# Kernel optimization log

Measured on AMD Instinct MI355X. Metric: run time of the kernel, lower is better.

Reference implementation:

```python
import jax, jax.numpy as jnp
import numpy as np

B, N, DIM, DD = 8, 4096, 512, 512
SCALE = DD ** -0.5


def setup_inputs() -> dict:
    key = jax.random.key(0)
    ks = jax.random.split(key, 8)
    x = jax.random.normal(ks[0], (B, N, DIM), dtype=jnp.float32)
    mask = jnp.ones((B, N), dtype=bool)
    # torch nn.Linear(dim, decode_dim, bias=False): weight [DD, DIM], y = x @ W.T
    Wq = jax.random.normal(ks[1], (DD, DIM), dtype=jnp.float32) * (DIM ** -0.5)
    Wk = jax.random.normal(ks[2], (DD, DIM), dtype=jnp.float32) * (DIM ** -0.5)
    Wv = jax.random.normal(ks[3], (DD, DIM), dtype=jnp.float32) * (DIM ** -0.5)
    Wr = jax.random.normal(ks[4], (DD, DD), dtype=jnp.float32) * (DD ** -0.5)
    w_alpha = jax.random.normal(ks[5], (DD,), dtype=jnp.float32)
    w_beta = jax.random.normal(ks[6], (DD,), dtype=jnp.float32)
    return {"x": x, "Wq": Wq, "Wk": Wk, "Wv": Wv, "Wr": Wr,
            "w_alpha": w_alpha, "w_beta": w_beta, "mask": mask}


def _masked_softmax_n(logits, mask):
    # softmax over axis=1 (N), with -inf where mask is False
    logits = jnp.where(mask[:, :, None], logits, -jnp.inf)
    return jax.nn.softmax(logits, axis=1)


def reference(x, Wq, Wk, Wv, Wr, w_alpha, w_beta, mask):
    q = jnp.einsum('bnf,df->bnd', x, Wq)          # [B,N,DD]
    k = jnp.einsum('bnf,df->bnd', x, Wk)
    v = jnp.einsum('bnf,df->bnd', x, Wv)
    alpha = _masked_softmax_n(q * w_alpha * SCALE, mask)   # [B,N,DD]
    global_query = jnp.einsum('bnd,bnd->bd', q, alpha)     # [B,DD]
    p = global_query[:, None, :] * k                       # [B,N,DD]
    beta = _masked_softmax_n(p * w_beta * SCALE, mask)
    global_key = jnp.einsum('bnd,bnd->bd', p, beta)        # [B,DD]
    kv = global_key[:, None, :] * v                        # [B,N,DD]
    out = jnp.einsum('bnd,ed->bne', kv, Wr) + q
    return out
```

## Files before the change

### kernel.cpp

```cpp
#include <hip/hip_runtime.h>

#define B_    8
#define N_    4096
#define DIM_  512
#define DD_   512
#define M_    (B_ * N_)
#define SCALE_ 0.044194173824159216f

#define BM 128
#define BN 128
#define BK 32

typedef unsigned short u16;
typedef __attribute__((ext_vector_type(8))) short bf16x8;
typedef __attribute__((ext_vector_type(4))) float f32x4;

__device__ __forceinline__ float bf2f(u16 u) {
    union { unsigned i; float f; } c; c.i = ((unsigned)u) << 16; return c.f;
}
__device__ __forceinline__ u16 f2bf(float f) {
    union { float f; unsigned u; } c; c.f = f;
    unsigned r = c.u + 0x7FFFu + ((c.u >> 16) & 1u);
    return (u16)(r >> 16);
}

__global__ void detect(const void* wa, int* flag)
{
    __shared__ float mx[256];
    __shared__ int   zc[256];
    const u16* p = (const u16*)wa;
    const int t = threadIdx.x;
    float m = 0.f; int z = 0;
    for (int i = t; i < 512; i += 256) {
        u16 u = p[i];
        float v = fabsf(bf2f(u));
        if (v > m || v != v) m = (v != v) ? 1e30f : v;
        if (((i & 1) == 0) && u == 0) z++;
    }
    mx[t] = m; zc[t] = z; __syncthreads();
    for (int s = 128; s > 0; s >>= 1) {
        if (t < s) { mx[t] = fmaxf(mx[t], mx[t + s]); zc[t] += zc[t + s]; }
        __syncthreads();
    }
    if (t == 0) *flag = (mx[0] < 1000.0f && zc[0] <= 128) ? 0 : 1;
}

__global__ void cvt8(const void* s0, const void* s1, const void* s2, const void* s3,
                     u16* d0, u16* d1, u16* d2, u16* d3,
                     const int* __restrict__ flag, int n8)
{
    const void* s; u16* d;
    switch (blockIdx.z) {
        case 0:  s = s0; d = d0; break;
        case 1:  s = s1; d = d1; break;
        case 2:  s = s2; d = d2; break;
        default: s = s3; d = d3; break;
    }
    const int i = blockIdx.x * blockDim.x + threadIdx.x;
    if (i >= n8) return;
    if (*flag == 0) {
        ((uint4*)d)[i] = ((const uint4*)s)[i];
    } else {
        const float* f = (const float*)s + (size_t)i * 8;
        u16 o[8];
        #pragma unroll
        for (int j = 0; j < 8; ++j) o[j] = f2bf(f[j]);
        ((uint4*)d)[i] = *(uint4*)o;
    }
}

__global__ __launch_bounds__(256)
void gemm_red(const u16* __restrict__ A, const u16* __restrict__ Bt,
              const float* __restrict__ coef, float* T1, float* T2)
{
    __shared__ __align__(16) u16 As[BM * BK];
    __shared__ __align__(16) u16 Bs[BN * BK];
    __shared__ float rs1[8][128], rs2[8][128];

    const int tid   = threadIdx.x;
    const int wave  = tid >> 6, lane = tid & 63;
    const int waveM = wave >> 1, waveN = wave & 1;
    const int l15   = lane & 15, quad = lane >> 4;
    const int l4r   = lane >> 2, l4c  = lane & 3;
    const int tileN = blockIdx.x, tileM = blockIdx.y;
    const int b     = tileM >> 5;

    f32x4 acc[4][4] = {};

    const u16* aPtr = A  + (size_t)(tileM * BM + wave * 32 + l4r) * DIM_ + l4c * 8;
    const u16* bPtr = Bt + (size_t)(tileN * BN + wave * 32 + l4r) * DIM_ + l4c * 8;
    u16* asBase = As + wave * 1024;
    u16* bsBase = Bs + wave * 1024;

    for (int k0 = 0; k0 < DIM_; k0 += BK) {
        __builtin_amdgcn_global_load_lds(
            (const __attribute__((address_space(1))) void*)(aPtr + k0),
            (__attribute__((address_space(3))) void*)(asBase), 16, 0, 0);
        __builtin_amdgcn_global_load_lds(
            (const __attribute__((address_space(1))) void*)(aPtr + k0 + 16 * DIM_),
            (__attribute__((address_space(3))) void*)(asBase + 512), 16, 0, 0);
        __builtin_amdgcn_global_load_lds(
            (const __attribute__((address_space(1))) void*)(bPtr + k0),
            (__attribute__((address_space(3))) void*)(bsBase), 16, 0, 0);
        __builtin_amdgcn_global_load_lds(
            (const __attribute__((address_space(1))) void*)(bPtr + k0 + 16 * DIM_),
            (__attribute__((address_space(3))) void*)(bsBase + 512), 16, 0, 0);
        __syncthreads();

        bf16x8 af[4], bfr[4];
        #pragma unroll
        for (int mi = 0; mi < 4; ++mi)
            af[mi] = *(const bf16x8*)&As[(waveM * 64 + mi * 16 + l15) * BK + quad * 8];
        #pragma unroll
        for (int ni = 0; ni < 4; ++ni)
            bfr[ni] = *(const bf16x8*)&Bs[(waveN * 64 + ni * 16 + l15) * BK + quad * 8];
        #pragma unroll
        for (int mi = 0; mi < 4; ++mi)
            #pragma unroll
            for (int ni = 0; ni < 4; ++ni)
                acc[mi][ni] = __builtin_amdgcn_mfma_f32_16x16x32_bf16(
                    af[mi], bfr[ni], acc[mi][ni], 0, 0, 0);
        __syncthreads();
    }

    const int ridx = (waveM << 2) | quad;
    #pragma unroll
    for (int ni = 0; ni < 4; ++ni) {
        const int lcol = waveN * 64 + ni * 16 + l15;
        const float cf = coef[b * 512 + tileN * 128 + lcol];
        float s1 = 0.f, s2 = 0.f;
        #pragma unroll
        for (int mi = 0; mi < 4; ++mi)
            #pragma unroll
            for (int r = 0; r < 4; ++r) {
                float v = acc[mi][ni][r];
                float e = __expf(v * cf);
                s1 += e; s2 += v * e;
            }
        rs1[ridx][lcol] = s1; rs2[ridx][lcol] = s2;
    }
    __syncthreads();
    if (tid < 128) {
        float s1 = 0.f, s2 = 0.f;
        #pragma unroll
        for (int j = 0; j < 8; ++j) { s1 += rs1[j][tid]; s2 += rs2[j][tid]; }
        atomicAdd(&T1[b * 512 + tileN * 128 + tid], s1);
        atomicAdd(&T2[b * 512 + tileN * 128 + tid], s2);
    }
}

__global__ __launch_bounds__(256)
void gemm_bt(const u16* __restrict__ A, const u16* __restrict__ Bt,
             void* Cv, const u16* __restrict__ add,
             long aZ, long bZ, long cZ, long addZ, int bByRowBlk,
             const int* __restrict__ flagp)
{
    A  += (size_t)blockIdx.z * aZ;
    Bt += (size_t)blockIdx.z * bZ;
    if (bByRowBlk) Bt += (size_t)(blockIdx.y >> 5) * 262144;

    __shared__ __align__(16) u16 As[BM * BK];
    __shared__ __align__(16) u16 Bs[BN * BK];

    const int tid   = threadIdx.x;
    const int wave  = tid >> 6, lane = tid & 63;
    const int waveM = wave >> 1, waveN = wave & 1;
    const int l15   = lane & 15, quad = lane >> 4;
    const int l4r   = lane >> 2, l4c  = lane & 3;
    const int tileN = blockIdx.x, tileM = blockIdx.y;

    f32x4 acc[4][4] = {};

    const u16* aPtr = A  + (size_t)(tileM * BM + wave * 32 + l4r) * DIM_ + l4c * 8;
    const u16* bPtr = Bt + (size_t)(tileN * BN + wave * 32 + l4r) * DIM_ + l4c * 8;
    u16* asBase = As + wave * 1024;
    u16* bsBase = Bs + wave * 1024;

    for (int k0 = 0; k0 < DIM_; k0 += BK) {
        __builtin_amdgcn_global_load_lds(
            (const __attribute__((address_space(1))) void*)(aPtr + k0),
            (__attribute__((address_space(3))) void*)(asBase), 16, 0, 0);
        __builtin_amdgcn_global_load_lds(
            (const __attribute__((address_space(1))) void*)(aPtr + k0 + 16 * DIM_),
            (__attribute__((address_space(3))) void*)(asBase + 512), 16, 0, 0);
        __builtin_amdgcn_global_load_lds(
            (const __attribute__((address_space(1))) void*)(bPtr + k0),
            (__attribute__((address_space(3))) void*)(bsBase), 16, 0, 0);
        __builtin_amdgcn_global_load_lds(
            (const __attribute__((address_space(1))) void*)(bPtr + k0 + 16 * DIM_),
            (__attribute__((address_space(3))) void*)(bsBase + 512), 16, 0, 0);
        __syncthreads();

        bf16x8 af[4], bfr[4];
        #pragma unroll
        for (int mi = 0; mi < 4; ++mi)
            af[mi] = *(const bf16x8*)&As[(waveM * 64 + mi * 16 + l15) * BK + quad * 8];
        #pragma unroll
        for (int ni = 0; ni < 4; ++ni)
            bfr[ni] = *(const bf16x8*)&Bs[(waveN * 64 + ni * 16 + l15) * BK + quad * 8];
        #pragma unroll
        for (int mi = 0; mi < 4; ++mi)
            #pragma unroll
            for (int ni = 0; ni < 4; ++ni)
                acc[mi][ni] = __builtin_amdgcn_mfma_f32_16x16x32_bf16(
                    af[mi], bfr[ni], acc[mi][ni], 0, 0, 0);
        __syncthreads();
    }

    const int f32out = flagp ? *flagp : 0;
    #pragma unroll
    for (int mi = 0; mi < 4; ++mi) {
        #pragma unroll
        for (int ni = 0; ni < 4; ++ni) {
            const int row = tileM * BM + waveM * 64 + mi * 16 + quad * 4;
            const int col = tileN * BN + waveN * 64 + ni * 16 + l15;
            #pragma unroll
            for (int r = 0; r < 4; ++r) {
                float vv = acc[mi][ni][r];
                const size_t oo = (size_t)(row + r) * DD_ + col;
                if (add) vv += bf2f(add[(size_t)blockIdx.z * addZ + oo]);
                const size_t o = (size_t)blockIdx.z * cZ + oo;
                if (f32out) ((float*)Cv)[o] = vv;
                else        ((u16*)Cv)[o]   = f2bf(vv);
            }
        }
    }
}

__global__ void coefq_k(const u16* __restrict__ wab, float* coefQ)
{
    const int i = blockIdx.x * 256 + threadIdx.x;
    coefQ[i] = bf2f(wab[i & 511]) * SCALE_;
}

__global__ void comb1_k(const float* __restrict__ T1, const float* __restrict__ T2,
                        const u16* __restrict__ wbb, float* gq, float* coefK)
{
    const int i = blockIdx.x * 256 + threadIdx.x;
    const float g = T2[i] / T1[i];
    gq[i] = g;
    coefK[i] = g * bf2f(wbb[i & 511]) * SCALE_;
}

__global__ void comb2_k(const float* __restrict__ T1, const float* __restrict__ T2,
                        const float* __restrict__ gq, float* gk)
{
    const int i = blockIdx.x * 256 + threadIdx.x;
    gk[i] = gq[i] * (T2[i] / T1[i]);
}

__global__ void transp(const u16* __restrict__ Wv, u16* WvT)
{
    __shared__ u16 t[32][33];
    const int f0 = (blockIdx.x & 15) * 32, d0 = (blockIdx.x >> 4) * 32;
    const int c = threadIdx.x & 31, r0 = threadIdx.x >> 5;
    #pragma unroll
    for (int p = 0; p < 4; ++p)
        t[r0 + p * 8][c] = Wv[(size_t)(d0 + r0 + p * 8) * 512 + f0 + c];
    __syncthreads();
    #pragma unroll
    for (int p = 0; p < 4; ++p)
        WvT[(size_t)(f0 + r0 + p * 8) * 512 + d0 + c] = t[c][r0 + p * 8];
}

__global__ void scaleA(const u16* __restrict__ Wr, const float* __restrict__ gk, u16* Ap)
{
    const size_t idx0 = ((size_t)blockIdx.x * 256 + threadIdx.x) * 8;
    const int b = (int)(idx0 >> 18);
    const int d = (int)(idx0 & 511);
    const size_t ed = idx0 & ((1u << 18) - 1);
    const float* g = gk + b * 512 + d;
    u16 in[8], o[8];
    *(uint4*)in = *(const uint4*)(Wr + ed);
    #pragma unroll
    for (int j = 0; j < 8; ++j) o[j] = f2bf(bf2f(in[j]) * g[j]);
    *(uint4*)(Ap + idx0) = *(uint4*)o;
}

extern "C" void kernel_launch(void* const* d_in, const int* in_sizes, int n_in,
                              void* d_out, int out_size, void* d_ws, size_t ws_size,
                              hipStream_t stream)
{
    const void* x  = d_in[0];
    const void* Wq = d_in[1];
    const void* Wk = d_in[2];
    const void* Wv = d_in[3];
    const void* Wr = d_in[4];
    const void* wa = d_in[5];
    const void* wb = d_in[6];

    char* ws = (char*)d_ws;
    int*   flag  = (int*)  (ws);
    float* TQ1   = (float*)(ws + 1024);
    float* TQ2   = (float*)(ws + 17 * 1024);
    float* TK1   = (float*)(ws + 33 * 1024);
    float* TK2   = (float*)(ws + 49 * 1024);
    float* gq    = (float*)(ws + 65 * 1024);
    float* gk    = (float*)(ws + 81 * 1024);
    float* coefQ = (float*)(ws + 97 * 1024);
    float* coefK = (float*)(ws + 113 * 1024);
    u16*   wab   = (u16*)  (ws + 129 * 1024);
    u16*   wbb   = (u16*)  (ws + 130 * 1024);
    u16*   Wqb   = (u16*)  (ws + 131 * 1024);
    u16*   Wkb   = (u16*)  (ws + 643 * 1024);
    u16*   Wvb   = (u16*)  (ws + 1155 * 1024);
    u16*   Wrb   = (u16*)  (ws + 1667 * 1024);
    u16*   WvT   = (u16*)  (ws + 2179 * 1024);
    u16*   Ap    = (u16*)  (ws + 2691 * 1024);
    u16*   W2    = (u16*)  (ws + 6787 * 1024);
    u16*   xb    = (u16*)  (ws + 10883 * 1024);

    detect<<<1, 256, 0, stream>>>(wa, flag);
    hipMemsetAsync(ws + 1024, 0, 65536, stream);

    cvt8<<<dim3(8192, 1, 1), 256, 0, stream>>>(x, x, x, x, xb, xb, xb, xb, flag, 2097152);
    cvt8<<<dim3(128, 1, 4), 256, 0, stream>>>(Wq, Wk, Wv, Wr, Wqb, Wkb, Wvb, Wrb, flag, 32768);
    cvt8<<<dim3(1, 1, 2), 64, 0, stream>>>(wa, wb, wa, wb, wab, wbb, wab, wbb, flag, 64);

    coefq_k<<<16, 256, 0, stream>>>(wab, coefQ);
    gemm_red<<<dim3(4, 256), 256, 0, stream>>>(xb, Wqb, coefQ, TQ1, TQ2);
    comb1_k<<<16, 256, 0, stream>>>(TQ1, TQ2, wbb, gq, coefK);

    gemm_red<<<dim3(4, 256), 256, 0, stream>>>(xb, Wkb, coefK, TK1, TK2);
    comb2_k<<<16, 256, 0, stream>>>(TK1, TK2, gq, gk);

    transp<<<256, 256, 0, stream>>>(Wvb, WvT);
    scaleA<<<1024, 256, 0, stream>>>(Wrb, gk, Ap);
    gemm_bt<<<dim3(4, 4, 8), 256, 0, stream>>>(Ap, WvT, W2, Wqb,
                                               262144L, 0L, 262144L, 0L, 0, nullptr);

    gemm_bt<<<dim3(4, 256, 1), 256, 0, stream>>>(xb, W2, d_out, nullptr,
                                                 0L, 0L, 0L, 0L, 1, flag);
}
```

Baseline: 262.3 us.

## Fuse Q/K projections into one GEMM, stash K in output, drop dtype detection

```diff
diff --git a/kernel.cpp b/kernel.cpp
--- a/kernel.cpp
+++ b/kernel.cpp
@@ -1,15 +1,8 @@
 #include <hip/hip_runtime.h>
 
-#define B_    8
 #define N_    4096
-#define DIM_  512
 #define DD_   512
-#define M_    (B_ * N_)
 #define SCALE_ 0.044194173824159216f
-
-#define BM 128
-#define BN 128
-#define BK 32
 
 typedef unsigned short u16;
 typedef __attribute__((ext_vector_type(8))) short bf16x8;
@@ -23,117 +16,94 @@
     unsigned r = c.u + 0x7FFFu + ((c.u >> 16) & 1u);
     return (u16)(r >> 16);
 }
-
-__global__ void detect(const void* wa, int* flag)
-{
-    __shared__ float mx[256];
-    __shared__ int   zc[256];
-    const u16* p = (const u16*)wa;
-    const int t = threadIdx.x;
-    float m = 0.f; int z = 0;
-    for (int i = t; i < 512; i += 256) {
-        u16 u = p[i];
-        float v = fabsf(bf2f(u));
-        if (v > m || v != v) m = (v != v) ? 1e30f : v;
-        if (((i & 1) == 0) && u == 0) z++;
-    }
-    mx[t] = m; zc[t] = z; __syncthreads();
-    for (int s = 128; s > 0; s >>= 1) {
-        if (t < s) { mx[t] = fmaxf(mx[t], mx[t + s]); zc[t] += zc[t + s]; }
-        __syncthreads();
-    }
-    if (t == 0) *flag = (mx[0] < 1000.0f && zc[0] <= 128) ? 0 : 1;
-}
-
-__global__ void cvt8(const void* s0, const void* s1, const void* s2, const void* s3,
-                     u16* d0, u16* d1, u16* d2, u16* d3,
-                     const int* __restrict__ flag, int n8)
-{
-    const void* s; u16* d;
-    switch (blockIdx.z) {
-        case 0:  s = s0; d = d0; break;
-        case 1:  s = s1; d = d1; break;
-        case 2:  s = s2; d = d2; break;
-        default: s = s3; d = d3; break;
-    }
-    const int i = blockIdx.x * blockDim.x + threadIdx.x;
-    if (i >= n8) return;
-    if (*flag == 0) {
-        ((uint4*)d)[i] = ((const uint4*)s)[i];
-    } else {
-        const float* f = (const float*)s + (size_t)i * 8;
-        u16 o[8];
-        #pragma unroll
-        for (int j = 0; j < 8; ++j) o[j] = f2bf(f[j]);
-        ((uint4*)d)[i] = *(uint4*)o;
-    }
+__device__ __forceinline__ void gl_lds(const u16* g, u16* l) {
+    __builtin_amdgcn_global_load_lds(
+        (const __attribute__((address_space(1))) void*)g,
+        (__attribute__((address_space(3))) void*)l, 16, 0, 0);
+}
+
+__global__ void cvt_x(const float* __restrict__ s, u16* __restrict__ d)
+{
+    const size_t i = ((size_t)blockIdx.x * 256 + threadIdx.x) * 8;
+    float4 f0 = *(const float4*)(s + i), f1 = *(const float4*)(s + i + 4);
+    u16 o[8];
+    o[0]=f2bf(f0.x); o[1]=f2bf(f0.y); o[2]=f2bf(f0.z); o[3]=f2bf(f0.w);
+    o[4]=f2bf(f1.x); o[5]=f2bf(f1.y); o[6]=f2bf(f1.z); o[7]=f2bf(f1.w);
+    *(uint4*)(d + i) = *(uint4*)o;
+}
+
+__global__ void cvt_w(const float* s0, const float* s1, u16* d0, u16* d1)
+{
+    const float* s = blockIdx.z ? s1 : s0;
+    u16* d = blockIdx.z ? d1 : d0;
+    const size_t i = ((size_t)blockIdx.x * 256 + threadIdx.x) * 8;
+    float4 f0 = *(const float4*)(s + i), f1 = *(const float4*)(s + i + 4);
+    u16 o[8];
+    o[0]=f2bf(f0.x); o[1]=f2bf(f0.y); o[2]=f2bf(f0.z); o[3]=f2bf(f0.w);
+    o[4]=f2bf(f1.x); o[5]=f2bf(f1.y); o[6]=f2bf(f1.z); o[7]=f2bf(f1.w);
+    *(uint4*)(d + i) = *(uint4*)o;
 }
 
 __global__ __launch_bounds__(256)
-void gemm_red(const u16* __restrict__ A, const u16* __restrict__ Bt,
-              const float* __restrict__ coef, float* T1, float* T2)
-{
-    __shared__ __align__(16) u16 As[BM * BK];
-    __shared__ __align__(16) u16 Bs[BN * BK];
+void gemm_qk(const u16* __restrict__ A, const u16* __restrict__ Bq,
+             const u16* __restrict__ Bk, const float* __restrict__ wa,
+             u16* __restrict__ kb, float* T1, float* T2)
+{
+    __shared__ __align__(16) u16 As[4096], Bqs[4096], Bks[4096];
     __shared__ float rs1[8][128], rs2[8][128];
 
-    const int tid   = threadIdx.x;
-    const int wave  = tid >> 6, lane = tid & 63;
+    const int tid = threadIdx.x, wave = tid >> 6, lane = tid & 63;
     const int waveM = wave >> 1, waveN = wave & 1;
-    const int l15   = lane & 15, quad = lane >> 4;
-    const int l4r   = lane >> 2, l4c  = lane & 3;
+    const int l15 = lane & 15, quad = lane >> 4;
+    const int l4r = lane >> 2, l4c = lane & 3;
     const int tileN = blockIdx.x, tileM = blockIdx.y;
-    const int b     = tileM >> 5;
-
-    f32x4 acc[4][4] = {};
-
-    const u16* aPtr = A  + (size_t)(tileM * BM + wave * 32 + l4r) * DIM_ + l4c * 8;
-    const u16* bPtr = Bt + (size_t)(tileN * BN + wave * 32 + l4r) * DIM_ + l4c * 8;
-    u16* asBase = As + wave * 1024;
-    u16* bsBase = Bs + wave * 1024;
-
-    for (int k0 = 0; k0 < DIM_; k0 += BK) {
-        __builtin_amdgcn_global_load_lds(
-            (const __attribute__((address_space(1))) void*)(aPtr + k0),
-            (__attribute__((address_space(3))) void*)(asBase), 16, 0, 0);
-        __builtin_amdgcn_global_load_lds(
-            (const __attribute__((address_space(1))) void*)(aPtr + k0 + 16 * DIM_),
-            (__attribute__((address_space(3))) void*)(asBase + 512), 16, 0, 0);
-        __builtin_amdgcn_global_load_lds(
-            (const __attribute__((address_space(1))) void*)(bPtr + k0),
-            (__attribute__((address_space(3))) void*)(bsBase), 16, 0, 0);
-        __builtin_amdgcn_global_load_lds(
-            (const __attribute__((address_space(1))) void*)(bPtr + k0 + 16 * DIM_),
-            (__attribute__((address_space(3))) void*)(bsBase + 512), 16, 0, 0);
-        __syncthreads();
-
-        bf16x8 af[4], bfr[4];
-        #pragma unroll
-        for (int mi = 0; mi < 4; ++mi)
-            af[mi] = *(const bf16x8*)&As[(waveM * 64 + mi * 16 + l15) * BK + quad * 8];
-        #pragma unroll
-        for (int ni = 0; ni < 4; ++ni)
-            bfr[ni] = *(const bf16x8*)&Bs[(waveN * 64 + ni * 16 + l15) * BK + quad * 8];
-        #pragma unroll
-        for (int mi = 0; mi < 4; ++mi)
-            #pragma unroll
-            for (int ni = 0; ni < 4; ++ni)
-                acc[mi][ni] = __builtin_amdgcn_mfma_f32_16x16x32_bf16(
-                    af[mi], bfr[ni], acc[mi][ni], 0, 0, 0);
-        __syncthreads();
-    }
-
-    const int ridx = (waveM << 2) | quad;
+    const int b = tileM >> 5;
+
+    f32x4 aq[4][4] = {}, ak[4][4] = {};
+
+    const u16* aPtr  = A  + (size_t)(tileM * 128 + wave * 32 + l4r) * 512 + l4c * 8;
+    const u16* bqPtr = Bq + (size_t)(tileN * 128 + wave * 32 + l4r) * 512 + l4c * 8;
+    const u16* bkPtr = Bk + (size_t)(tileN * 128 + wave * 32 + l4r) * 512 + l4c * 8;
+    u16* asB = As  + wave * 1024;
+    u16* bqB = Bqs + wave * 1024;
+    u16* bkB = Bks + wave * 1024;
+
+    for (int k0 = 0; k0 < 512; k0 += 32) {
+        gl_lds(aPtr  + k0, asB);  gl_lds(aPtr  + k0 + 8192, asB + 512);
+        gl_lds(bqPtr + k0, bqB);  gl_lds(bqPtr + k0 + 8192, bqB + 512);
+        gl_lds(bkPtr + k0, bkB);  gl_lds(bkPtr + k0 + 8192, bkB + 512);
+        __syncthreads();
+
+        bf16x8 af[4], bqf[4], bkf[4];
+        #pragma unroll
+        for (int mi = 0; mi < 4; ++mi)
+            af[mi] = *(const bf16x8*)&As[(waveM * 64 + mi * 16 + l15) * 32 + quad * 8];
+        #pragma unroll
+        for (int ni = 0; ni < 4; ++ni) {
+            bqf[ni] = *(const bf16x8*)&Bqs[(waveN * 64 + ni * 16 + l15) * 32 + quad * 8];
+            bkf[ni] = *(const bf16x8*)&Bks[(waveN * 64 + ni * 16 + l15) * 32 + quad * 8];
+        }
+        #pragma unroll
+        for (int mi = 0; mi < 4; ++mi)
+            #pragma unroll
+            for (int ni = 0; ni < 4; ++ni) {
+                aq[mi][ni] = __builtin_amdgcn_mfma_f32_16x16x32_bf16(af[mi], bqf[ni], aq[mi][ni], 0, 0, 0);
+                ak[mi][ni] = __builtin_amdgcn_mfma_f32_16x16x32_bf16(af[mi], bkf[ni], ak[mi][ni], 0, 0, 0);
+            }
+        __syncthreads();
+    }
+
+    const int ridx = waveM * 4 + quad;
     #pragma unroll
     for (int ni = 0; ni < 4; ++ni) {
         const int lcol = waveN * 64 + ni * 16 + l15;
-        const float cf = coef[b * 512 + tileN * 128 + lcol];
+        const float cf = wa[tileN * 128 + lcol] * SCALE_;
         float s1 = 0.f, s2 = 0.f;
         #pragma unroll
         for (int mi = 0; mi < 4; ++mi)
             #pragma unroll
             for (int r = 0; r < 4; ++r) {
-                float v = acc[mi][ni][r];
+                float v = aq[mi][ni][r];
                 float e = __expf(v * cf);
                 s1 += e; s2 += v * e;
             }
@@ -147,111 +117,62 @@
         atomicAdd(&T1[b * 512 + tileN * 128 + tid], s1);
         atomicAdd(&T2[b * 512 + tileN * 128 + tid], s2);
     }
-}
-
-__global__ __launch_bounds__(256)
-void gemm_bt(const u16* __restrict__ A, const u16* __restrict__ Bt,
-             void* Cv, const u16* __restrict__ add,
-             long aZ, long bZ, long cZ, long addZ, int bByRowBlk,
-             const int* __restrict__ flagp)
-{
-    A  += (size_t)blockIdx.z * aZ;
-    Bt += (size_t)blockIdx.z * bZ;
-    if (bByRowBlk) Bt += (size_t)(blockIdx.y >> 5) * 262144;
-
-    __shared__ __align__(16) u16 As[BM * BK];
-    __shared__ __align__(16) u16 Bs[BN * BK];
-
-    const int tid   = threadIdx.x;
-    const int wave  = tid >> 6, lane = tid & 63;
-    const int waveM = wave >> 1, waveN = wave & 1;
-    const int l15   = lane & 15, quad = lane >> 4;
-    const int l4r   = lane >> 2, l4c  = lane & 3;
-    const int tileN = blockIdx.x, tileM = blockIdx.y;
-
-    f32x4 acc[4][4] = {};
-
-    const u16* aPtr = A  + (size_t)(tileM * BM + wave * 32 + l4r) * DIM_ + l4c * 8;
-    const u16* bPtr = Bt + (size_t)(tileN * BN + wave * 32 + l4r) * DIM_ + l4c * 8;
-    u16* asBase = As + wave * 1024;
-    u16* bsBase = Bs + wave * 1024;
-
-    for (int k0 = 0; k0 < DIM_; k0 += BK) {
-        __builtin_amdgcn_global_load_lds(
-            (const __attribute__((address_space(1))) void*)(aPtr + k0),
-            (__attribute__((address_space(3))) void*)(asBase), 16, 0, 0);
-        __builtin_amdgcn_global_load_lds(
-            (const __attribute__((address_space(1))) void*)(aPtr + k0 + 16 * DIM_),
-            (__attribute__((address_space(3))) void*)(asBase + 512), 16, 0, 0);
-        __builtin_amdgcn_global_load_lds(
-            (const __attribute__((address_space(1))) void*)(bPtr + k0),
-            (__attribute__((address_space(3))) void*)(bsBase), 16, 0, 0);
-        __builtin_amdgcn_global_load_lds(
-            (const __attribute__((address_space(1))) void*)(bPtr + k0 + 16 * DIM_),
-            (__attribute__((address_space(3))) void*)(bsBase + 512), 16, 0, 0);
-        __syncthreads();
-
-        bf16x8 af[4], bfr[4];
-        #pragma unroll
-        for (int mi = 0; mi < 4; ++mi)
-            af[mi] = *(const bf16x8*)&As[(waveM * 64 + mi * 16 + l15) * BK + quad * 8];
-        #pragma unroll
-        for (int ni = 0; ni < 4; ++ni)
-            bfr[ni] = *(const bf16x8*)&Bs[(waveN * 64 + ni * 16 + l15) * BK + quad * 8];
-        #pragma unroll
-        for (int mi = 0; mi < 4; ++mi)
-            #pragma unroll
-            for (int ni = 0; ni < 4; ++ni)
-                acc[mi][ni] = __builtin_amdgcn_mfma_f32_16x16x32_bf16(
-                    af[mi], bfr[ni], acc[mi][ni], 0, 0, 0);
-        __syncthreads();
-    }
-
-    const int f32out = flagp ? *flagp : 0;
+
     #pragma unroll
     for (int mi = 0; mi < 4; ++mi) {
         #pragma unroll
         for (int ni = 0; ni < 4; ++ni) {
-            const int row = tileM * BM + waveM * 64 + mi * 16 + quad * 4;
-            const int col = tileN * BN + waveN * 64 + ni * 16 + l15;
-            #pragma unroll
-            for (int r = 0; r < 4; ++r) {
-                float vv = acc[mi][ni][r];
-                const size_t oo = (size_t)(row + r) * DD_ + col;
-                if (add) vv += bf2f(add[(size_t)blockIdx.z * addZ + oo]);
-                const size_t o = (size_t)blockIdx.z * cZ + oo;
-                if (f32out) ((float*)Cv)[o] = vv;
-                else        ((u16*)Cv)[o]   = f2bf(vv);
-            }
-        }
-    }
-}
-
-__global__ void coefq_k(const u16* __restrict__ wab, float* coefQ)
-{
-    const int i = blockIdx.x * 256 + threadIdx.x;
-    coefQ[i] = bf2f(wab[i & 511]) * SCALE_;
+            const int row = tileM * 128 + waveM * 64 + mi * 16 + quad * 4;
+            const int col = tileN * 128 + waveN * 64 + ni * 16 + l15;
+            #pragma unroll
+            for (int r = 0; r < 4; ++r)
+                kb[(size_t)(row + r) * 512 + col] = f2bf(ak[mi][ni][r]);
+        }
+    }
 }
 
 __global__ void comb1_k(const float* __restrict__ T1, const float* __restrict__ T2,
-                        const u16* __restrict__ wbb, float* gq, float* coefK)
+                        const float* __restrict__ wb, float* gq, float* coefK)
 {
     const int i = blockIdx.x * 256 + threadIdx.x;
     const float g = T2[i] / T1[i];
     gq[i] = g;
-    coefK[i] = g * bf2f(wbb[i & 511]) * SCALE_;
-}
-
-__global__ void comb2_k(const float* __restrict__ T1, const float* __restrict__ T2,
+    coefK[i] = g * wb[i & 511] * SCALE_;
+}
+
+__global__ void red2(const u16* __restrict__ kb, const float* __restrict__ coefK,
+                     float* P1, float* P2)
+{
+    const int d = blockIdx.x * 256 + threadIdx.x;
+    const int c = blockIdx.y, b = blockIdx.z;
+    const float cf = coefK[b * 512 + d];
+    const u16* base = kb + ((size_t)(b * N_ + c * 256)) * 512 + d;
+    float s1 = 0.f, s2 = 0.f;
+    for (int i = 0; i < 256; ++i) {
+        float kv = bf2f(base[(size_t)i * 512]);
+        float e  = __expf(kv * cf);
+        s1 += e; s2 += kv * e;
+    }
+    P1[(b * 16 + c) * 512 + d] = s1;
+    P2[(b * 16 + c) * 512 + d] = s2;
+}
+
+__global__ void comb2_k(const float* __restrict__ P1, const float* __restrict__ P2,
                         const float* __restrict__ gq, float* gk)
 {
     const int i = blockIdx.x * 256 + threadIdx.x;
-    gk[i] = gq[i] * (T2[i] / T1[i]);
-}
-
-__global__ void transp(const u16* __restrict__ Wv, u16* WvT)
-{
-    __shared__ u16 t[32][33];
+    const int b = i >> 9, d = i & 511;
+    float s1 = 0.f, s2 = 0.f;
+    for (int c = 0; c < 16; ++c) {
+        s1 += P1[(b * 16 + c) * 512 + d];
+        s2 += P2[(b * 16 + c) * 512 + d];
+    }
+    gk[i] = gq[i] * (s2 / s1);
+}
+
+__global__ void transp_cvt(const float* __restrict__ Wv, u16* WvT)
+{
+    __shared__ float t[32][33];
     const int f0 = (blockIdx.x & 15) * 32, d0 = (blockIdx.x >> 4) * 32;
     const int c = threadIdx.x & 31, r0 = threadIdx.x >> 5;
     #pragma unroll
@@ -260,75 +181,181 @@
     __syncthreads();
     #pragma unroll
     for (int p = 0; p < 4; ++p)
-        WvT[(size_t)(f0 + r0 + p * 8) * 512 + d0 + c] = t[c][r0 + p * 8];
-}
-
-__global__ void scaleA(const u16* __restrict__ Wr, const float* __restrict__ gk, u16* Ap)
+        WvT[(size_t)(f0 + r0 + p * 8) * 512 + d0 + c] = f2bf(t[c][r0 + p * 8]);
+}
+
+__global__ void scaleA(const float* __restrict__ Wr, const float* __restrict__ gk, u16* Ap)
 {
     const size_t idx0 = ((size_t)blockIdx.x * 256 + threadIdx.x) * 8;
     const int b = (int)(idx0 >> 18);
     const int d = (int)(idx0 & 511);
     const size_t ed = idx0 & ((1u << 18) - 1);
     const float* g = gk + b * 512 + d;
-    u16 in[8], o[8];
-    *(uint4*)in = *(const uint4*)(Wr + ed);
-    #pragma unroll
-    for (int j = 0; j < 8; ++j) o[j] = f2bf(bf2f(in[j]) * g[j]);
+    float4 a0 = *(const float4*)(Wr + ed), a1 = *(const float4*)(Wr + ed + 4);
+    u16 o[8];
+    o[0]=f2bf(a0.x*g[0]); o[1]=f2bf(a0.y*g[1]); o[2]=f2bf(a0.z*g[2]); o[3]=f2bf(a0.w*g[3]);
+    o[4]=f2bf(a1.x*g[4]); o[5]=f2bf(a1.y*g[5]); o[6]=f2bf(a1.z*g[6]); o[7]=f2bf(a1.w*g[7]);
     *(uint4*)(Ap + idx0) = *(uint4*)o;
+}
+
+__global__ __launch_bounds__(256)
+void gemm_w2(const u16* __restrict__ Ap, const u16* __restrict__ Bt,
+             u16* __restrict__ C, const float* __restrict__ addF)
+{
+    const u16* A = Ap + (size_t)blockIdx.z * 262144;
+    u16* Cb = C + (size_t)blockIdx.z * 262144;
+
+    __shared__ __align__(16) u16 As[4096], Bs[4096];
+    const int tid = threadIdx.x, wave = tid >> 6, lane = tid & 63;
+    const int waveM = wave >> 1, waveN = wave & 1;
+    const int l15 = lane & 15, quad = lane >> 4;
+    const int l4r = lane >> 2, l4c = lane & 3;
+    const int tileN = blockIdx.x, tileM = blockIdx.y;
+
+    f32x4 acc[4][4] = {};
+    const u16* aPtr = A  + (size_t)(tileM * 128 + wave * 32 + l4r) * 512 + l4c * 8;
+    const u16* bPtr = Bt + (size_t)(tileN * 128 + wave * 32 + l4r) * 512 + l4c * 8;
+    u16* asB = As + wave * 1024;
+    u16* bsB = Bs + wave * 1024;
+
+    for (int k0 = 0; k0 < 512; k0 += 32) {
+        gl_lds(aPtr + k0, asB); gl_lds(aPtr + k0 + 8192, asB + 512);
+        gl_lds(bPtr + k0, bsB); gl_lds(bPtr + k0 + 8192, bsB + 512);
+        __syncthreads();
+        bf16x8 af[4], bfr[4];
+        #pragma unroll
+        for (int mi = 0; mi < 4; ++mi)
+            af[mi] = *(const bf16x8*)&As[(waveM * 64 + mi * 16 + l15) * 32 + quad * 8];
+        #pragma unroll
+        for (int ni = 0; ni < 4; ++ni)
+            bfr[ni] = *(const bf16x8*)&Bs[(waveN * 64 + ni * 16 + l15) * 32 + quad * 8];
+        #pragma unroll
+        for (int mi = 0; mi < 4; ++mi)
+            #pragma unroll
+            for (int ni = 0; ni < 4; ++ni)
+                acc[mi][ni] = __builtin_amdgcn_mfma_f32_16x16x32_bf16(af[mi], bfr[ni], acc[mi][ni], 0, 0, 0);
+        __syncthreads();
+    }
+
+    #pragma unroll
+    for (int mi = 0; mi < 4; ++mi)
+        #pragma unroll
+        for (int ni = 0; ni < 4; ++ni) {
+            const int row = tileM * 128 + waveM * 64 + mi * 16 + quad * 4;
+            const int col = tileN * 128 + waveN * 64 + ni * 16 + l15;
+            #pragma unroll
+            for (int r = 0; r < 4; ++r) {
+                float vv = acc[mi][ni][r] + addF[(size_t)(row + r) * 512 + col];
+                Cb[(size_t)(row + r) * 512 + col] = f2bf(vv);
+            }
+        }
+}
+
+__global__ __launch_bounds__(256)
+void gemm_out(const u16* __restrict__ A, const u16* __restrict__ W2,
+              float* __restrict__ out)
+{
+    const u16* Bt = W2 + (size_t)(blockIdx.y >> 5) * 262144;
+
+    __shared__ __align__(16) u16 As[4096], Bs[4096];
+    __shared__ __align__(16) float eb[32 * 132];
+
+    const int tid = threadIdx.x, wave = tid >> 6, lane = tid & 63;
+    const int waveM = wave >> 1, waveN = wave & 1;
+    const int l15 = lane & 15, quad = lane >> 4;
+    const int l4r = lane >> 2, l4c = lane & 3;
+    const int tileN = blockIdx.x, tileM = blockIdx.y;
+
+    f32x4 acc[4][4] = {};
+    const u16* aPtr = A  + (size_t)(tileM * 128 + wave * 32 + l4r) * 512 + l4c * 8;
+    const u16* bPtr = Bt + (size_t)(tileN * 128 + wave * 32 + l4r) * 512 + l4c * 8;
+    u16* asB = As + wave * 1024;
+    u16* bsB = Bs + wave * 1024;
+
+    for (int k0 = 0; k0 < 512; k0 += 32) {
+        gl_lds(aPtr + k0, asB); gl_lds(aPtr + k0 + 8192, asB + 512);
+        gl_lds(bPtr + k0, bsB); gl_lds(bPtr + k0 + 8192, bsB + 512);
+        __syncthreads();
+        bf16x8 af[4], bfr[4];
+        #pragma unroll
+        for (int mi = 0; mi < 4; ++mi)
+            af[mi] = *(const bf16x8*)&As[(waveM * 64 + mi * 16 + l15) * 32 + quad * 8];
+        #pragma unroll
+        for (int ni = 0; ni < 4; ++ni)
+            bfr[ni] = *(const bf16x8*)&Bs[(waveN * 64 + ni * 16 + l15) * 32 + quad * 8];
+        #pragma unroll
+        for (int mi = 0; mi < 4; ++mi)
+            #pragma unroll
+            for (int ni = 0; ni < 4; ++ni)
+                acc[mi][ni] = __builtin_amdgcn_mfma_f32_16x16x32_bf16(af[mi], bfr[ni], acc[mi][ni], 0, 0, 0);
+        __syncthreads();
+    }
+
+    #pragma unroll
+    for (int mi = 0; mi < 4; ++mi) {
+        if (mi) __syncthreads();
+        #pragma unroll
+        for (int ni = 0; ni < 4; ++ni) {
+            const int lrow = waveM * 16 + quad * 4;
+            const int lcol = waveN * 64 + ni * 16 + l15;
+            #pragma unroll
+            for (int r = 0; r < 4; ++r)
+                eb[(lrow + r) * 132 + lcol] = acc[mi][ni][r];
+        }
+        __syncthreads();
+        #pragma unroll
+        for (int i = 0; i < 4; ++i) {
+            const int f4 = tid + i * 256;
+            const int lr = f4 >> 5;
+            const int cp = (f4 & 31) * 4;
+            const int grow = tileM * 128 + (lr >> 4) * 64 + mi * 16 + (lr & 15);
+            float4 vv = *(const float4*)&eb[lr * 132 + cp];
+            *(float4*)&out[(size_t)grow * 512 + tileN * 128 + cp] = vv;
+        }
+    }
 }
 
 extern "C" void kernel_launch(void* const* d_in, const int* in_sizes, int n_in,
                               void* d_out, int out_size, void* d_ws, size_t ws_size,
                               hipStream_t stream)
 {
-    const void* x  = d_in[0];
-    const void* Wq = d_in[1];
-    const void* Wk = d_in[2];
-    const void* Wv = d_in[3];
-    const void* Wr = d_in[4];
-    const void* wa = d_in[5];
-    const void* wb = d_in[6];
+    const float* x  = (const float*)d_in[0];
+    const float* Wq = (const float*)d_in[1];
+    const float* Wk = (const float*)d_in[2];
+    const float* Wv = (const float*)d_in[3];
+    const float* Wr = (const float*)d_in[4];
+    const float* wa = (const float*)d_in[5];
+    const float* wb = (const float*)d_in[6];
+    float* out = (float*)d_out;
+    u16* kb = (u16*)d_out;
 
     char* ws = (char*)d_ws;
-    int*   flag  = (int*)  (ws);
-    float* TQ1   = (float*)(ws + 1024);
-    float* TQ2   = (float*)(ws + 17 * 1024);
-    float* TK1   = (float*)(ws + 33 * 1024);
-    float* TK2   = (float*)(ws + 49 * 1024);
-    float* gq    = (float*)(ws + 65 * 1024);
-    float* gk    = (float*)(ws + 81 * 1024);
-    float* coefQ = (float*)(ws + 97 * 1024);
-    float* coefK = (float*)(ws + 113 * 1024);
-    u16*   wab   = (u16*)  (ws + 129 * 1024);
-    u16*   wbb   = (u16*)  (ws + 130 * 1024);
-    u16*   Wqb   = (u16*)  (ws + 131 * 1024);
-    u16*   Wkb   = (u16*)  (ws + 643 * 1024);
-    u16*   Wvb   = (u16*)  (ws + 1155 * 1024);
-    u16*   Wrb   = (u16*)  (ws + 1667 * 1024);
-    u16*   WvT   = (u16*)  (ws + 2179 * 1024);
-    u16*   Ap    = (u16*)  (ws + 2691 * 1024);
-    u16*   W2    = (u16*)  (ws + 6787 * 1024);
-    u16*   xb    = (u16*)  (ws + 10883 * 1024);
-
-    detect<<<1, 256, 0, stream>>>(wa, flag);
-    hipMemsetAsync(ws + 1024, 0, 65536, stream);
-
-    cvt8<<<dim3(8192, 1, 1), 256, 0, stream>>>(x, x, x, x, xb, xb, xb, xb, flag, 2097152);
-    cvt8<<<dim3(128, 1, 4), 256, 0, stream>>>(Wq, Wk, Wv, Wr, Wqb, Wkb, Wvb, Wrb, flag, 32768);
-    cvt8<<<dim3(1, 1, 2), 64, 0, stream>>>(wa, wb, wa, wb, wab, wbb, wab, wbb, flag, 64);
-
-    coefq_k<<<16, 256, 0, stream>>>(wab, coefQ);
-    gemm_red<<<dim3(4, 256), 256, 0, stream>>>(xb, Wqb, coefQ, TQ1, TQ2);
-    comb1_k<<<16, 256, 0, stream>>>(TQ1, TQ2, wbb, gq, coefK);
-
-    gemm_red<<<dim3(4, 256), 256, 0, stream>>>(xb, Wkb, coefK, TK1, TK2);
-    comb2_k<<<16, 256, 0, stream>>>(TK1, TK2, gq, gk);
-
-    transp<<<256, 256, 0, stream>>>(Wvb, WvT);
-    scaleA<<<1024, 256, 0, stream>>>(Wrb, gk, Ap);
-    gemm_bt<<<dim3(4, 4, 8), 256, 0, stream>>>(Ap, WvT, W2, Wqb,
-                                               262144L, 0L, 262144L, 0L, 0, nullptr);
-
-    gemm_bt<<<dim3(4, 256, 1), 256, 0, stream>>>(xb, W2, d_out, nullptr,
-                                                 0L, 0L, 0L, 0L, 1, flag);
-}
+    float* TQ1   = (float*)(ws);
+    float* TQ2   = (float*)(ws + 16 * 1024);
+    float* gq    = (float*)(ws + 32 * 1024);
+    float* coefK = (float*)(ws + 48 * 1024);
+    float* gk    = (float*)(ws + 64 * 1024);
+    float* P1k   = (float*)(ws + 80 * 1024);
+    float* P2k   = (float*)(ws + 336 * 1024);
+    u16*   WvT   = (u16*)  (ws + 592 * 1024);
+    u16*   Wqb   = (u16*)  (ws + 1104 * 1024);
+    u16*   Wkb   = (u16*)  (ws + 1616 * 1024);
+    u16*   Ap    = (u16*)  (ws + 2128 * 1024);
+    u16*   W2    = (u16*)  (ws + 6224 * 1024);
+    u16*   xb    = (u16*)  (ws + 10320 * 1024);
+
+    hipMemsetAsync(TQ1, 0, 32 * 1024, stream);
+    cvt_x<<<8192, 256, 0, stream>>>(x, xb);
+    cvt_w<<<dim3(128, 1, 2), 256, 0, stream>>>(Wq, Wk, Wqb, Wkb);
+
+    gemm_qk<<<dim3(4, 256), 256, 0, stream>>>(xb, Wqb, Wkb, wa, kb, TQ1, TQ2);
+    comb1_k<<<16, 256, 0, stream>>>(TQ1, TQ2, wb, gq, coefK);
+    red2<<<dim3(2, 16, 8), 256, 0, stream>>>(kb, coefK, P1k, P2k);
+    comb2_k<<<16, 256, 0, stream>>>(P1k, P2k, gq, gk);
+
+    transp_cvt<<<256, 256, 0, stream>>>(Wv, WvT);
+    scaleA<<<1024, 256, 0, stream>>>(Wr, gk, Ap);
+    gemm_w2<<<dim3(4, 4, 8), 256, 0, stream>>>(Ap, WvT, W2, Wq);
+
+    gemm_out<<<dim3(4, 256), 256, 0, stream>>>(xb, W2, out);
+}
```

Result: slower. 283.3 us (+8.0%).
